# Kernel optimization log

Hardware: AMD Instinct MI355X
Metric: run time of the kernel (lower is better)

The kernel has to match this reference:

```python
import jax, jax.numpy as jnp
import numpy as np

N_NODES = 10000
N_EDGES = 80000
IN_DIM = 1024
HID = 4096
OUT = 256


def sage_conv(x, src, dst, W_l, b_l, W_r, num_nodes):
    # mean aggregation of source-node features onto target nodes
    msg = x[src]                                            # [E, D] gather
    agg = jax.ops.segment_sum(msg, dst, num_segments=num_nodes)   # [N, D]
    cnt = jax.ops.segment_sum(jnp.ones((src.shape[0],), x.dtype), dst,
                              num_segments=num_nodes)       # [N]
    mean = agg / jnp.clip(cnt, 1.0)[:, None]                # isolated nodes -> 0
    # lin_l(mean) + lin_r(x); lin_r has no bias in PyG SAGEConv
    return mean @ W_l.T + b_l + x @ W_r.T


def setup_inputs() -> dict:
    key = jax.random.key(0)
    ks = jax.random.split(key, 6)
    x = jax.random.normal(ks[0], (N_NODES, IN_DIM), dtype=jnp.float32)
    edge_index = jax.random.randint(ks[1], (2, N_EDGES), 0, N_NODES, dtype=jnp.int32)
    s1 = 1.0 / np.sqrt(IN_DIM)
    s2 = 1.0 / np.sqrt(HID)
    W1_l = jax.random.normal(ks[2], (HID, IN_DIM), dtype=jnp.float32) * s1
    b1_l = jnp.zeros((HID,), jnp.float32)
    W1_r = jax.random.normal(ks[3], (HID, IN_DIM), dtype=jnp.float32) * s1
    W2_l = jax.random.normal(ks[4], (OUT, HID), dtype=jnp.float32) * s2
    b2_l = jnp.zeros((OUT,), jnp.float32)
    W2_r = jax.random.normal(ks[5], (OUT, HID), dtype=jnp.float32) * s2
    return {"x": x, "edge_index": edge_index, "W1_l": W1_l, "b1_l": b1_l,
            "W1_r": W1_r, "W2_l": W2_l, "b2_l": b2_l, "W2_r": W2_r}


def reference(x, edge_index, W1_l, b1_l, W1_r, W2_l, b2_l, W2_r):
    src, dst = edge_index[0], edge_index[1]
    h = sage_conv(x, src, dst, W1_l, b1_l, W1_r, N_NODES)   # [N, 4096]
    h = jax.nn.relu(h)
    # dropout is identity in eval mode
    out = sage_conv(h, src, dst, W2_l, b2_l, W2_r, N_NODES)  # [N, 256]
    return jax.nn.log_softmax(out, axis=1)
```

## Files before the change

kernel.cpp:

```cpp
#include <hip/hip_runtime.h>
#include <cstdint>
#include <cstddef>

#define DEVINL __device__ __forceinline__

typedef __bf16 bf16x8 __attribute__((ext_vector_type(8)));
typedef float f32x4 __attribute__((ext_vector_type(4)));

static constexpr int NN = 10000;
static constexpr int NE = 80000;
static constexpr int IN_DIM = 1024;
static constexpr int HID = 4096;
static constexpr int OUTD = 256;
static constexpr int M_PAD = 10112;

DEVINL unsigned short f2bf(float f) {
  unsigned int u = __builtin_bit_cast(unsigned int, f);
  u += 0x7fffu + ((u >> 16) & 1u);
  return (unsigned short)(u >> 16);
}
DEVINL float bf2f(unsigned short h) {
  unsigned int u = ((unsigned int)h) << 16;
  return __builtin_bit_cast(float, u);
}

DEVINL void ld_lds16(const void* g, void* l) {
  __builtin_amdgcn_global_load_lds(
      (const __attribute__((address_space(1))) unsigned int*)g,
      (__attribute__((address_space(3))) unsigned int*)l, 16, 0, 0);
}

static constexpr int PREP_B1 = 8192;
static constexpr int PREP_B2 = PREP_B1 + 2048;
static constexpr int PREP_B3 = PREP_B2 + 10000;
static constexpr int PREP_NB = PREP_B3 + 313;

__global__ __launch_bounds__(256) void prep_kernel(
    const float* __restrict__ W1l, const float* __restrict__ W1r,
    const float* __restrict__ W2l, const float* __restrict__ W2r,
    const float* __restrict__ x, const int* __restrict__ dst,
    unsigned short* __restrict__ w1cat, unsigned short* __restrict__ w2cat,
    unsigned short* __restrict__ x_bf, int* __restrict__ deg) {
  int b = blockIdx.x;
  int t = threadIdx.x;
  if (b < PREP_B1) {
    int g = b * 256 + t;
    int n = g >> 9;
    int kg = g & 511;
    const float* s = (kg < 256) ? (W1l + (size_t)n * 1024 + kg * 4)
                                : (W1r + (size_t)n * 1024 + (kg - 256) * 4);
    float4 v = *(const float4*)s;
    ushort4 p = {f2bf(v.x), f2bf(v.y), f2bf(v.z), f2bf(v.w)};
    ((ushort4*)w1cat)[g] = p;
  } else if (b < PREP_B2) {
    int g = (b - PREP_B1) * 256 + t;
    int n = g >> 10;
    int kg = g & 1023;
    const float* s = (n < 256) ? (W2l + (size_t)n * 4096 + kg * 4)
                               : (W2r + (size_t)(n - 256) * 4096 + kg * 4);
    float4 v = *(const float4*)s;
    ushort4 p = {f2bf(v.x), f2bf(v.y), f2bf(v.z), f2bf(v.w)};
    ((ushort4*)w2cat)[g] = p;
  } else if (b < PREP_B3) {
    int g = (b - PREP_B2) * 256 + t;
    int i = g >> 8;
    int kg = g & 255;
    float4 v = ((const float4*)(x + (size_t)i * IN_DIM))[kg];
    ushort4 p = {f2bf(v.x), f2bf(v.y), f2bf(v.z), f2bf(v.w)};
    ((ushort4*)(x_bf + (size_t)i * IN_DIM))[kg] = p;
  } else {
    int e = (b - PREP_B3) * 256 + t;
    if (e < NE) atomicAdd(&deg[dst[e]], 1);
  }
}

__global__ __launch_bounds__(256) void scan_kernel(const int* __restrict__ deg,
                                                   int* __restrict__ offs,
                                                   int* __restrict__ cur) {
  __shared__ int part[256];
  constexpr int NPT = 40;
  int t = threadIdx.x;
  int base = t * NPT;
  int s = 0;
  for (int j = 0; j < NPT; ++j) {
    int n = base + j;
    s += (n < NN) ? deg[n] : 0;
  }
  part[t] = s;
  __syncthreads();
  for (int o = 1; o < 256; o <<= 1) {
    int v = (t >= o) ? part[t - o] : 0;
    __syncthreads();
    part[t] += v;
    __syncthreads();
  }
  int pre = (t > 0) ? part[t - 1] : 0;
  for (int j = 0; j < NPT; ++j) {
    int n = base + j;
    if (n < NN) {
      offs[n] = pre;
      cur[n] = pre;
      pre += deg[n];
    }
  }
  if (t == 255) offs[NN] = part[255];
}

__global__ void bin_kernel(const int* __restrict__ src, const int* __restrict__ dst,
                           int* __restrict__ cur, int* __restrict__ csr) {
  int e = blockIdx.x * 256 + threadIdx.x;
  if (e < NE) {
    int p = atomicAdd(&cur[dst[e]], 1);
    csr[p] = src[e];
  }
}

__global__ __launch_bounds__(256) void gather1_kernel(const unsigned short* __restrict__ x_bf,
                                                      const int* __restrict__ offs,
                                                      const int* __restrict__ csr,
                                                      unsigned short* __restrict__ A1) {
  int i = blockIdx.x;
  int t = threadIdx.x;
  unsigned short* row = A1 + (size_t)i * 2048;
  if (i >= NN) {
    ushort4 z = {0, 0, 0, 0};
    ((ushort4*)row)[t] = z;
    ((ushort4*)(row + 1024))[t] = z;
    return;
  }
  int beg = offs[i], end = offs[i + 1];
  float4 a0 = {0.f, 0.f, 0.f, 0.f}, a1 = {0.f, 0.f, 0.f, 0.f};
  int j = beg;
  for (; j + 2 <= end; j += 2) {
    int s0 = __builtin_amdgcn_readfirstlane(csr[j]);
    int s1 = __builtin_amdgcn_readfirstlane(csr[j + 1]);
    ushort4 u0 = ((const ushort4*)(x_bf + (size_t)s0 * IN_DIM))[t];
    ushort4 u1 = ((const ushort4*)(x_bf + (size_t)s1 * IN_DIM))[t];
    a0.x += bf2f(u0.x); a0.y += bf2f(u0.y); a0.z += bf2f(u0.z); a0.w += bf2f(u0.w);
    a1.x += bf2f(u1.x); a1.y += bf2f(u1.y); a1.z += bf2f(u1.z); a1.w += bf2f(u1.w);
  }
  if (j < end) {
    int s0 = __builtin_amdgcn_readfirstlane(csr[j]);
    ushort4 u0 = ((const ushort4*)(x_bf + (size_t)s0 * IN_DIM))[t];
    a0.x += bf2f(u0.x); a0.y += bf2f(u0.y); a0.z += bf2f(u0.z); a0.w += bf2f(u0.w);
  }
  float inv = 1.0f / (float)max(end - beg, 1);
  ushort4 ub = ((const ushort4*)(x_bf + (size_t)i * IN_DIM))[t];
  ushort4 pa = {f2bf((a0.x + a1.x) * inv), f2bf((a0.y + a1.y) * inv),
                f2bf((a0.z + a1.z) * inv), f2bf((a0.w + a1.w) * inv)};
  ((ushort4*)row)[t] = pa;
  ((ushort4*)(row + 1024))[t] = ub;
}

template <int BM, int BN, int BK, int K, int KSPLIT, int N, int NUMM, int NUMN, int GM,
          int EPI, int NWY>
__global__ __launch_bounds__(256) void gemm_kernel(const unsigned short* __restrict__ A,
                                                   const unsigned short* __restrict__ Bt,
                                                   const float* __restrict__ bias,
                                                   void* __restrict__ C0out) {
  constexpr int MGR = 4 / NWY;
  constexpr int MI = BM / 16 / MGR;
  constexpr int NI = 4;
  constexpr int CPR = BK / 8;
  constexpr int SA = BM * CPR / 256;
  constexpr int SB = BN * CPR / 256;
  constexpr int KK = BK / 32;
  constexpr int KS = K / KSPLIT;
  __shared__ unsigned short Asm[BM * BK];
  __shared__ unsigned short Bsm[BN * BK];

  constexpr int NPG = GM * NUMN;
  const int pid = blockIdx.x;
  const int gid = pid / NPG;
  const int first_m = gid * GM;
  const int sz = (NUMM - first_m < GM) ? (NUMM - first_m) : GM;
  const int local = pid % NPG;
  const int pm = first_m + local % sz;
  const int pn = local / sz;
  const int koff = (KSPLIT > 1) ? (int)blockIdx.y * KS : 0;

  const int tid = threadIdx.x;
  const int lane = tid & 63;
  const int wave = tid >> 6;
  const int quad = lane >> 4;
  const int l16 = lane & 15;
  const int wm = (wave % MGR) * (BM / MGR);
  const int wn = (wave / MGR) * 64;
  const long tm0 = (long)pm * BM;
  const long tn0 = (long)pn * BN;

  f32x4 acc[MI][NI];
#pragma unroll
  for (int i = 0; i < MI; ++i)
#pragma unroll
    for (int j = 0; j < NI; ++j) acc[i][j] = (f32x4){0.f, 0.f, 0.f, 0.f};

  const unsigned short* aSrc[SA];
  unsigned short* aDst[SA];
  const unsigned short* bSrc[SB];
  unsigned short* bDst[SB];
#pragma unroll
  for (int s = 0; s < SA; ++s) {
    int c = s * 256 + wave * 64 + lane;
    int r = c / CPR;
    int g = (c % CPR) ^ (r & 7);
    aSrc[s] = A + (size_t)(tm0 + r) * K + koff + g * 8;
    aDst[s] = Asm + s * 2048 + wave * 512;
  }
#pragma unroll
  for (int s = 0; s < SB; ++s) {
    int c = s * 256 + wave * 64 + lane;
    int r = c / CPR;
    int g = (c % CPR) ^ (r & 7);
    bSrc[s] = Bt + (size_t)(tn0 + r) * K + koff + g * 8;
    bDst[s] = Bsm + s * 2048 + wave * 512;
  }

  const int l7 = l16 & 7;

  for (int k0 = 0; k0 < KS; k0 += BK) {
#pragma unroll
    for (int s = 0; s < SA; ++s) ld_lds16(aSrc[s] + k0, aDst[s]);
#pragma unroll
    for (int s = 0; s < SB; ++s) ld_lds16(bSrc[s] + k0, bDst[s]);
    __syncthreads();

#pragma unroll
    for (int kk = 0; kk < KK; ++kk) {
      const int p = (kk * 4 + quad) ^ l7;
      bf16x8 af[MI], bv[NI];
#pragma unroll
      for (int i = 0; i < MI; ++i) {
        int ra = wm + i * 16 + l16;
        af[i] = *(const bf16x8*)(Asm + ra * BK + p * 8);
      }
#pragma unroll
      for (int j = 0; j < NI; ++j) {
        int rb = wn + j * 16 + l16;
        bv[j] = *(const bf16x8*)(Bsm + rb * BK + p * 8);
      }
#pragma unroll
      for (int i = 0; i < MI; ++i)
#pragma unroll
        for (int j = 0; j < NI; ++j)
          acc[i][j] = __builtin_amdgcn_mfma_f32_16x16x32_bf16(af[i], bv[j], acc[i][j], 0, 0, 0);
    }
    __syncthreads();
  }

  if (EPI == 1) {
    unsigned short* C = (unsigned short*)C0out;
#pragma unroll
    for (int i = 0; i < MI; ++i) {
      long m0 = tm0 + wm + i * 16 + quad * 4;
#pragma unroll
      for (int j = 0; j < NI; ++j) {
        int n = (int)tn0 + wn + j * 16 + l16;
        float bvs = bias[n];
#pragma unroll
        for (int r = 0; r < 4; ++r) {
          float v = acc[i][j][r] + bvs;
          v = fmaxf(v, 0.0f);
          C[(size_t)(m0 + r) * N + n] = f2bf(v);
        }
      }
    }
  } else {
    unsigned short* C = (unsigned short*)C0out + (size_t)blockIdx.y * NUMM * BM * N;
#pragma unroll
    for (int i = 0; i < MI; ++i) {
      long m0 = tm0 + wm + i * 16 + quad * 4;
#pragma unroll
      for (int j = 0; j < NI; ++j) {
        int n = (int)tn0 + wn + j * 16 + l16;
#pragma unroll
        for (int r = 0; r < 4; ++r) C[(size_t)(m0 + r) * N + n] = f2bf(acc[i][j][r]);
      }
    }
  }
}

__global__ __launch_bounds__(256) void reduce2_kernel(const unsigned short* __restrict__ P,
                                                      unsigned short* __restrict__ pl,
                                                      float* __restrict__ pr) {
  int tid = threadIdx.x;
  size_t row = (size_t)blockIdx.x * 4 + (tid >> 6);
  int col = (tid & 63) * 8;
  size_t base = row * 512 + col;
  uint4 a = *(const uint4*)(P + base);
  uint4 b = *(const uint4*)(P + (size_t)M_PAD * 512 + base);
  float s[8];
  const unsigned int* aw = (const unsigned int*)&a;
  const unsigned int* bw = (const unsigned int*)&b;
#pragma unroll
  for (int j = 0; j < 4; ++j) {
    s[2 * j] = bf2f((unsigned short)(aw[j] & 0xffffu)) + bf2f((unsigned short)(bw[j] & 0xffffu));
    s[2 * j + 1] = bf2f((unsigned short)(aw[j] >> 16)) + bf2f((unsigned short)(bw[j] >> 16));
  }
  if (col < 256) {
    unsigned int o[4];
#pragma unroll
    for (int j = 0; j < 4; ++j)
      o[j] = (unsigned int)f2bf(s[2 * j]) | ((unsigned int)f2bf(s[2 * j + 1]) << 16);
    *(uint4*)(pl + row * 256 + col) = *(const uint4*)o;
  } else {
    float* d = pr + row * 256 + (col - 256);
    *(float4*)d = (float4){s[0], s[1], s[2], s[3]};
    *(float4*)(d + 4) = (float4){s[4], s[5], s[6], s[7]};
  }
}

__global__ __launch_bounds__(128) void gather2_final_kernel(const unsigned short* __restrict__ pl,
                                                            const float* __restrict__ pr,
                                                            const int* __restrict__ offs,
                                                            const int* __restrict__ csr,
                                                            const float* __restrict__ b2,
                                                            float* __restrict__ out) {
  int i = blockIdx.x;
  int t = threadIdx.x;
  int beg = offs[i], end = offs[i + 1];
  float a0 = 0.f, a1 = 0.f, c0 = 0.f, c1 = 0.f;
  int j = beg;
  for (; j + 2 <= end; j += 2) {
    int s0 = __builtin_amdgcn_readfirstlane(csr[j]);
    int s1 = __builtin_amdgcn_readfirstlane(csr[j + 1]);
    unsigned int u0 = ((const unsigned int*)(pl + (size_t)s0 * 256))[t];
    unsigned int u1 = ((const unsigned int*)(pl + (size_t)s1 * 256))[t];
    a0 += bf2f((unsigned short)(u0 & 0xffffu));
    a1 += bf2f((unsigned short)(u0 >> 16));
    c0 += bf2f((unsigned short)(u1 & 0xffffu));
    c1 += bf2f((unsigned short)(u1 >> 16));
  }
  if (j < end) {
    int s0 = __builtin_amdgcn_readfirstlane(csr[j]);
    unsigned int u0 = ((const unsigned int*)(pl + (size_t)s0 * 256))[t];
    a0 += bf2f((unsigned short)(u0 & 0xffffu));
    a1 += bf2f((unsigned short)(u0 >> 16));
  }
  float inv = 1.0f / (float)max(end - beg, 1);
  float2 bv = ((const float2*)b2)[t];
  float2 pv = ((const float2*)(pr + (size_t)i * 256))[t];
  float v0 = (a0 + c0) * inv + bv.x + pv.x;
  float v1 = (a1 + c1) * inv + bv.y + pv.y;

  __shared__ float sm[2], ss[2];
  int w = t >> 6;
  float m = fmaxf(v0, v1);
#pragma unroll
  for (int o = 32; o > 0; o >>= 1) m = fmaxf(m, __shfl_xor(m, o, 64));
  if ((t & 63) == 0) sm[w] = m;
  __syncthreads();
  m = fmaxf(sm[0], sm[1]);

  float s = __expf(v0 - m) + __expf(v1 - m);
#pragma unroll
  for (int o = 32; o > 0; o >>= 1) s += __shfl_xor(s, o, 64);
  if ((t & 63) == 0) ss[w] = s;
  __syncthreads();
  float ls = logf(ss[0] + ss[1]);

  float2 o2 = {v0 - m - ls, v1 - m - ls};
  ((float2*)(out + (size_t)i * OUTD))[t] = o2;
}

static constexpr size_t OFF_A1 = 0;
static constexpr size_t OFF_W1 = OFF_A1 + (size_t)M_PAD * 2048 * 2;
static constexpr size_t OFF_HB = OFF_W1 + (size_t)HID * 2048 * 2;
static constexpr size_t OFF_W2 = OFF_HB + (size_t)M_PAD * HID * 2;
static constexpr size_t OFF_XBF = OFF_W2 - (size_t)NN * IN_DIM * 2;
static constexpr size_t OFF_DEG = OFF_W2 + (size_t)512 * HID * 2;
static constexpr size_t OFF_OFFS = OFF_DEG + (size_t)NN * 4;
static constexpr size_t OFF_CUR = OFF_OFFS + (size_t)(NN + 4) * 4;
static constexpr size_t OFF_CSR = OFF_CUR + (size_t)NN * 4;
static constexpr size_t OFF_P = OFF_A1;
static constexpr size_t OFF_PL = OFF_P + (size_t)2 * M_PAD * 512 * 2;
static constexpr size_t OFF_PR = OFF_PL + (size_t)M_PAD * 256 * 2;

extern "C" void kernel_launch(void* const* d_in, const int* in_sizes, int n_in,
                              void* d_out, int out_size, void* d_ws, size_t ws_size,
                              hipStream_t stream) {
  const float* x = (const float*)d_in[0];
  const int* ei = (const int*)d_in[1];
  const int* src = ei;
  const int* dst = ei + NE;
  const float* W1_l = (const float*)d_in[2];
  const float* b1_l = (const float*)d_in[3];
  const float* W1_r = (const float*)d_in[4];
  const float* W2_l = (const float*)d_in[5];
  const float* b2_l = (const float*)d_in[6];
  const float* W2_r = (const float*)d_in[7];
  float* out = (float*)d_out;

  char* ws = (char*)d_ws;
  unsigned short* A1 = (unsigned short*)(ws + OFF_A1);
  unsigned short* w1cat = (unsigned short*)(ws + OFF_W1);
  unsigned short* h_b = (unsigned short*)(ws + OFF_HB);
  unsigned short* x_bf = (unsigned short*)(ws + OFF_XBF);
  unsigned short* w2cat = (unsigned short*)(ws + OFF_W2);
  int* deg = (int*)(ws + OFF_DEG);
  int* offs = (int*)(ws + OFF_OFFS);
  int* cur = (int*)(ws + OFF_CUR);
  int* csr = (int*)(ws + OFF_CSR);
  unsigned short* P = (unsigned short*)(ws + OFF_P);
  unsigned short* pl = (unsigned short*)(ws + OFF_PL);
  float* pr = (float*)(ws + OFF_PR);

  hipMemsetAsync(deg, 0, (size_t)NN * 4, stream);

  prep_kernel<<<PREP_NB, 256, 0, stream>>>(W1_l, W1_r, W2_l, W2_r, x, dst,
                                           w1cat, w2cat, x_bf, deg);
  scan_kernel<<<1, 256, 0, stream>>>(deg, offs, cur);
  bin_kernel<<<(NE + 255) / 256, 256, 0, stream>>>(src, dst, cur, csr);

  gather1_kernel<<<M_PAD, 256, 0, stream>>>(x_bf, offs, csr, A1);

  gemm_kernel<128, 128, 64, 2048, 1, 4096, 79, 32, 32, 1, 2>
      <<<79 * 32, 256, 0, stream>>>(A1, w1cat, b1_l, h_b);
  gemm_kernel<64, 256, 64, 4096, 2, 512, 158, 2, 1, 3, 4>
      <<<dim3(158 * 2, 2), 256, 0, stream>>>(h_b, w2cat, nullptr, P);
  reduce2_kernel<<<M_PAD / 4, 256, 0, stream>>>(P, pl, pr);

  gather2_final_kernel<<<NN, 128, 0, stream>>>(pl, pr, offs, csr, b2_l, out);
}
```

Baseline: 441.5 us.

## Read GEMM1 A operand from two buffers, fold split-K reduce into gather2

The first GEMM now loads its A operand from two separate buffers: the aggregated mean for the first half of K and the bf16 copy of x for the second half. This removes the copy of x into a concatenated A1 buffer inside gather1. The reduce2 kernel is dropped, and gather2_final reads and sums both split-K partial buffers directly, which costs twice as many gathered loads per edge. The scan kernel also moves to 1024 threads, and the x_bf padding rows are zeroed in gather1.

After: 437.7 us. Within noise of the previous version (-0.9%).

```diff
diff --git a/kernel.cpp b/kernel.cpp
--- a/kernel.cpp
+++ b/kernel.cpp
@@ -74,11 +74,11 @@
   }
 }
 
-__global__ __launch_bounds__(256) void scan_kernel(const int* __restrict__ deg,
-                                                   int* __restrict__ offs,
-                                                   int* __restrict__ cur) {
-  __shared__ int part[256];
-  constexpr int NPT = 40;
+__global__ __launch_bounds__(1024) void scan_kernel(const int* __restrict__ deg,
+                                                    int* __restrict__ offs,
+                                                    int* __restrict__ cur) {
+  __shared__ int part[1024];
+  constexpr int NPT = 10;
   int t = threadIdx.x;
   int base = t * NPT;
   int s = 0;
@@ -88,7 +88,7 @@
   }
   part[t] = s;
   __syncthreads();
-  for (int o = 1; o < 256; o <<= 1) {
+  for (int o = 1; o < 1024; o <<= 1) {
     int v = (t >= o) ? part[t - o] : 0;
     __syncthreads();
     part[t] += v;
@@ -103,7 +103,7 @@
       pre += deg[n];
     }
   }
-  if (t == 255) offs[NN] = part[255];
+  if (t == 1023) offs[NN] = part[1023];
 }
 
 __global__ void bin_kernel(const int* __restrict__ src, const int* __restrict__ dst,
@@ -115,17 +115,17 @@
   }
 }
 
-__global__ __launch_bounds__(256) void gather1_kernel(const unsigned short* __restrict__ x_bf,
+__global__ __launch_bounds__(256) void gather1_kernel(unsigned short* __restrict__ x_bf,
                                                       const int* __restrict__ offs,
                                                       const int* __restrict__ csr,
                                                       unsigned short* __restrict__ A1) {
   int i = blockIdx.x;
   int t = threadIdx.x;
-  unsigned short* row = A1 + (size_t)i * 2048;
+  unsigned short* row = A1 + (size_t)i * 1024;
   if (i >= NN) {
     ushort4 z = {0, 0, 0, 0};
     ((ushort4*)row)[t] = z;
-    ((ushort4*)(row + 1024))[t] = z;
+    ((ushort4*)(x_bf + (size_t)i * 1024))[t] = z;
     return;
   }
   int beg = offs[i], end = offs[i + 1];
@@ -145,16 +145,15 @@
     a0.x += bf2f(u0.x); a0.y += bf2f(u0.y); a0.z += bf2f(u0.z); a0.w += bf2f(u0.w);
   }
   float inv = 1.0f / (float)max(end - beg, 1);
-  ushort4 ub = ((const ushort4*)(x_bf + (size_t)i * IN_DIM))[t];
   ushort4 pa = {f2bf((a0.x + a1.x) * inv), f2bf((a0.y + a1.y) * inv),
                 f2bf((a0.z + a1.z) * inv), f2bf((a0.w + a1.w) * inv)};
   ((ushort4*)row)[t] = pa;
-  ((ushort4*)(row + 1024))[t] = ub;
 }
 
 template <int BM, int BN, int BK, int K, int KSPLIT, int N, int NUMM, int NUMN, int GM,
-          int EPI, int NWY>
+          int EPI, int NWY, bool ASPLIT>
 __global__ __launch_bounds__(256) void gemm_kernel(const unsigned short* __restrict__ A,
+                                                   const unsigned short* __restrict__ A2,
                                                    const unsigned short* __restrict__ Bt,
                                                    const float* __restrict__ bias,
                                                    void* __restrict__ C0out) {
@@ -166,6 +165,7 @@
   constexpr int SB = BN * CPR / 256;
   constexpr int KK = BK / 32;
   constexpr int KS = K / KSPLIT;
+  constexpr int AS = ASPLIT ? K / 2 : K;
   __shared__ unsigned short Asm[BM * BK];
   __shared__ unsigned short Bsm[BN * BK];
 
@@ -195,7 +195,7 @@
 #pragma unroll
     for (int j = 0; j < NI; ++j) acc[i][j] = (f32x4){0.f, 0.f, 0.f, 0.f};
 
-  const unsigned short* aSrc[SA];
+  size_t aOff[SA];
   unsigned short* aDst[SA];
   const unsigned short* bSrc[SB];
   unsigned short* bDst[SB];
@@ -204,7 +204,7 @@
     int c = s * 256 + wave * 64 + lane;
     int r = c / CPR;
     int g = (c % CPR) ^ (r & 7);
-    aSrc[s] = A + (size_t)(tm0 + r) * K + koff + g * 8;
+    aOff[s] = (size_t)(tm0 + r) * AS + koff + g * 8;
     aDst[s] = Asm + s * 2048 + wave * 512;
   }
 #pragma unroll
@@ -219,8 +219,10 @@
   const int l7 = l16 & 7;
 
   for (int k0 = 0; k0 < KS; k0 += BK) {
-#pragma unroll
-    for (int s = 0; s < SA; ++s) ld_lds16(aSrc[s] + k0, aDst[s]);
+    const unsigned short* ab = (!ASPLIT || k0 < K / 2) ? A : A2;
+    const int ka = ASPLIT ? (k0 & (K / 2 - 1)) : k0;
+#pragma unroll
+    for (int s = 0; s < SA; ++s) ld_lds16(ab + aOff[s] + ka, aDst[s]);
 #pragma unroll
     for (int s = 0; s < SB; ++s) ld_lds16(bSrc[s] + k0, bDst[s]);
     __syncthreads();
@@ -280,68 +282,44 @@
   }
 }
 
-__global__ __launch_bounds__(256) void reduce2_kernel(const unsigned short* __restrict__ P,
-                                                      unsigned short* __restrict__ pl,
-                                                      float* __restrict__ pr) {
-  int tid = threadIdx.x;
-  size_t row = (size_t)blockIdx.x * 4 + (tid >> 6);
-  int col = (tid & 63) * 8;
-  size_t base = row * 512 + col;
-  uint4 a = *(const uint4*)(P + base);
-  uint4 b = *(const uint4*)(P + (size_t)M_PAD * 512 + base);
-  float s[8];
-  const unsigned int* aw = (const unsigned int*)&a;
-  const unsigned int* bw = (const unsigned int*)&b;
-#pragma unroll
-  for (int j = 0; j < 4; ++j) {
-    s[2 * j] = bf2f((unsigned short)(aw[j] & 0xffffu)) + bf2f((unsigned short)(bw[j] & 0xffffu));
-    s[2 * j + 1] = bf2f((unsigned short)(aw[j] >> 16)) + bf2f((unsigned short)(bw[j] >> 16));
-  }
-  if (col < 256) {
-    unsigned int o[4];
-#pragma unroll
-    for (int j = 0; j < 4; ++j)
-      o[j] = (unsigned int)f2bf(s[2 * j]) | ((unsigned int)f2bf(s[2 * j + 1]) << 16);
-    *(uint4*)(pl + row * 256 + col) = *(const uint4*)o;
-  } else {
-    float* d = pr + row * 256 + (col - 256);
-    *(float4*)d = (float4){s[0], s[1], s[2], s[3]};
-    *(float4*)(d + 4) = (float4){s[4], s[5], s[6], s[7]};
-  }
-}
-
-__global__ __launch_bounds__(128) void gather2_final_kernel(const unsigned short* __restrict__ pl,
-                                                            const float* __restrict__ pr,
+__global__ __launch_bounds__(128) void gather2_final_kernel(const unsigned short* __restrict__ P,
                                                             const int* __restrict__ offs,
                                                             const int* __restrict__ csr,
                                                             const float* __restrict__ b2,
                                                             float* __restrict__ out) {
   int i = blockIdx.x;
   int t = threadIdx.x;
+  const unsigned short* P1 = P + (size_t)M_PAD * 512;
   int beg = offs[i], end = offs[i + 1];
   float a0 = 0.f, a1 = 0.f, c0 = 0.f, c1 = 0.f;
   int j = beg;
   for (; j + 2 <= end; j += 2) {
     int s0 = __builtin_amdgcn_readfirstlane(csr[j]);
     int s1 = __builtin_amdgcn_readfirstlane(csr[j + 1]);
-    unsigned int u0 = ((const unsigned int*)(pl + (size_t)s0 * 256))[t];
-    unsigned int u1 = ((const unsigned int*)(pl + (size_t)s1 * 256))[t];
-    a0 += bf2f((unsigned short)(u0 & 0xffffu));
-    a1 += bf2f((unsigned short)(u0 >> 16));
-    c0 += bf2f((unsigned short)(u1 & 0xffffu));
-    c1 += bf2f((unsigned short)(u1 >> 16));
+    unsigned int u0 = ((const unsigned int*)(P + (size_t)s0 * 512))[t];
+    unsigned int w0 = ((const unsigned int*)(P1 + (size_t)s0 * 512))[t];
+    unsigned int u1 = ((const unsigned int*)(P + (size_t)s1 * 512))[t];
+    unsigned int w1 = ((const unsigned int*)(P1 + (size_t)s1 * 512))[t];
+    a0 += bf2f((unsigned short)(u0 & 0xffffu)) + bf2f((unsigned short)(w0 & 0xffffu));
+    a1 += bf2f((unsigned short)(u0 >> 16)) + bf2f((unsigned short)(w0 >> 16));
+    c0 += bf2f((unsigned short)(u1 & 0xffffu)) + bf2f((unsigned short)(w1 & 0xffffu));
+    c1 += bf2f((unsigned short)(u1 >> 16)) + bf2f((unsigned short)(w1 >> 16));
   }
   if (j < end) {
     int s0 = __builtin_amdgcn_readfirstlane(csr[j]);
-    unsigned int u0 = ((const unsigned int*)(pl + (size_t)s0 * 256))[t];
-    a0 += bf2f((unsigned short)(u0 & 0xffffu));
-    a1 += bf2f((unsigned short)(u0 >> 16));
+    unsigned int u0 = ((const unsigned int*)(P + (size_t)s0 * 512))[t];
+    unsigned int w0 = ((const unsigned int*)(P1 + (size_t)s0 * 512))[t];
+    a0 += bf2f((unsigned short)(u0 & 0xffffu)) + bf2f((unsigned short)(w0 & 0xffffu));
+    a1 += bf2f((unsigned short)(u0 >> 16)) + bf2f((unsigned short)(w0 >> 16));
   }
   float inv = 1.0f / (float)max(end - beg, 1);
   float2 bv = ((const float2*)b2)[t];
-  float2 pv = ((const float2*)(pr + (size_t)i * 256))[t];
-  float v0 = (a0 + c0) * inv + bv.x + pv.x;
-  float v1 = (a1 + c1) * inv + bv.y + pv.y;
+  unsigned int su = ((const unsigned int*)(P + (size_t)i * 512))[128 + t];
+  unsigned int sw = ((const unsigned int*)(P1 + (size_t)i * 512))[128 + t];
+  float pv0 = bf2f((unsigned short)(su & 0xffffu)) + bf2f((unsigned short)(sw & 0xffffu));
+  float pv1 = bf2f((unsigned short)(su >> 16)) + bf2f((unsigned short)(sw >> 16));
+  float v0 = (a0 + c0) * inv + bv.x + pv0;
+  float v1 = (a1 + c1) * inv + bv.y + pv1;
 
   __shared__ float sm[2], ss[2];
   int w = t >> 6;
@@ -364,17 +342,15 @@
 }
 
 static constexpr size_t OFF_A1 = 0;
-static constexpr size_t OFF_W1 = OFF_A1 + (size_t)M_PAD * 2048 * 2;
+static constexpr size_t OFF_XBF = OFF_A1 + (size_t)M_PAD * 1024 * 2;
+static constexpr size_t OFF_W1 = OFF_XBF + (size_t)M_PAD * 1024 * 2;
 static constexpr size_t OFF_HB = OFF_W1 + (size_t)HID * 2048 * 2;
 static constexpr size_t OFF_W2 = OFF_HB + (size_t)M_PAD * HID * 2;
-static constexpr size_t OFF_XBF = OFF_W2 - (size_t)NN * IN_DIM * 2;
 static constexpr size_t OFF_DEG = OFF_W2 + (size_t)512 * HID * 2;
 static constexpr size_t OFF_OFFS = OFF_DEG + (size_t)NN * 4;
 static constexpr size_t OFF_CUR = OFF_OFFS + (size_t)(NN + 4) * 4;
 static constexpr size_t OFF_CSR = OFF_CUR + (size_t)NN * 4;
 static constexpr size_t OFF_P = OFF_A1;
-static constexpr size_t OFF_PL = OFF_P + (size_t)2 * M_PAD * 512 * 2;
-static constexpr size_t OFF_PR = OFF_PL + (size_t)M_PAD * 256 * 2;
 
 extern "C" void kernel_launch(void* const* d_in, const int* in_sizes, int n_in,
                               void* d_out, int out_size, void* d_ws, size_t ws_size,
@@ -393,32 +369,29 @@
 
   char* ws = (char*)d_ws;
   unsigned short* A1 = (unsigned short*)(ws + OFF_A1);
+  unsigned short* x_bf = (unsigned short*)(ws + OFF_XBF);
   unsigned short* w1cat = (unsigned short*)(ws + OFF_W1);
   unsigned short* h_b = (unsigned short*)(ws + OFF_HB);
-  unsigned short* x_bf = (unsigned short*)(ws + OFF_XBF);
   unsigned short* w2cat = (unsigned short*)(ws + OFF_W2);
   int* deg = (int*)(ws + OFF_DEG);
   int* offs = (int*)(ws + OFF_OFFS);
   int* cur = (int*)(ws + OFF_CUR);
   int* csr = (int*)(ws + OFF_CSR);
   unsigned short* P = (unsigned short*)(ws + OFF_P);
-  unsigned short* pl = (unsigned short*)(ws + OFF_PL);
-  float* pr = (float*)(ws + OFF_PR);
 
   hipMemsetAsync(deg, 0, (size_t)NN * 4, stream);
 
   prep_kernel<<<PREP_NB, 256, 0, stream>>>(W1_l, W1_r, W2_l, W2_r, x, dst,
                                            w1cat, w2cat, x_bf, deg);
-  scan_kernel<<<1, 256, 0, stream>>>(deg, offs, cur);
+  scan_kernel<<<1, 1024, 0, stream>>>(deg, offs, cur);
   bin_kernel<<<(NE + 255) / 256, 256, 0, stream>>>(src, dst, cur, csr);
 
   gather1_kernel<<<M_PAD, 256, 0, stream>>>(x_bf, offs, csr, A1);
 
-  gemm_kernel<128, 128, 64, 2048, 1, 4096, 79, 32, 32, 1, 2>
-      <<<79 * 32, 256, 0, stream>>>(A1, w1cat, b1_l, h_b);
-  gemm_kernel<64, 256, 64, 4096, 2, 512, 158, 2, 1, 3, 4>
-      <<<dim3(158 * 2, 2), 256, 0, stream>>>(h_b, w2cat, nullptr, P);
-  reduce2_kernel<<<M_PAD / 4, 256, 0, stream>>>(P, pl, pr);
-
-  gather2_final_kernel<<<NN, 128, 0, stream>>>(pl, pr, offs, csr, b2_l, out);
-}
+  gemm_kernel<128, 128, 64, 2048, 1, 4096, 79, 32, 32, 1, 2, true>
+      <<<79 * 32, 256, 0, stream>>>(A1, x_bf, w1cat, b1_l, h_b);
+  gemm_kernel<64, 256, 64, 4096, 2, 512, 158, 2, 1, 3, 4, false>
+      <<<dim3(158 * 2, 2), 256, 0, stream>>>(h_b, nullptr, w2cat, nullptr, P);
+
+  gather2_final_kernel<<<NN, 128, 0, stream>>>(P, offs, csr, b2_l, out);
+}
```
